# Performance work log

Measured on AMD Instinct MI355X. Metric: run time of the kernel, lower is better.

The kernel has to match this reference:

```python
import jax, jax.numpy as jnp
import numpy as np

EMBED = 1024
HEADS = 16
HEAD_DIM = EMBED // HEADS
B, S = 4, 1024


def setup_inputs() -> dict:
    key = jax.random.key(0)
    ks = jax.random.split(key, 8)
    return {
        "values": jax.random.normal(ks[0], (B, S, EMBED), dtype=jnp.float32),
        "keys": jax.random.normal(ks[1], (B, S, EMBED), dtype=jnp.float32),
        "query": jax.random.normal(ks[2], (B, S, EMBED), dtype=jnp.float32),
        "mask": jax.random.randint(ks[3], (B, 1, S, S), 0, 2, dtype=jnp.int32),
        "Wv": jax.random.normal(ks[4], (HEAD_DIM, HEAD_DIM), dtype=jnp.float32) / np.sqrt(HEAD_DIM),
        "Wq": jax.random.normal(ks[5], (HEAD_DIM, HEAD_DIM), dtype=jnp.float32) / np.sqrt(HEAD_DIM),
        "Wk": jax.random.normal(ks[6], (HEAD_DIM, HEAD_DIM), dtype=jnp.float32) / np.sqrt(HEAD_DIM),
        "Wu": jax.random.normal(ks[7], (EMBED, EMBED), dtype=jnp.float32) / np.sqrt(EMBED),
        "bu": jnp.zeros((EMBED,), dtype=jnp.float32),
    }


def reference(values, keys, query, mask, Wv, Wq, Wk, Wu, bu):
    n, s, _ = query.shape
    # split heads: [B, S, H, D]
    v = values.reshape(n, s, HEADS, HEAD_DIM)
    k = keys.reshape(n, s, HEADS, HEAD_DIM)
    q = query.reshape(n, s, HEADS, HEAD_DIM)
    # per-head linear (shared weight across heads); torch Linear: x @ W.T
    v = jnp.einsum("nshd,ed->nshe", v, Wv)
    k = jnp.einsum("nshd,ed->nshe", k, Wk)
    q = jnp.einsum("nshd,ed->nshe", q, Wq)
    # scores: [B, H, Q, K]
    dot = jnp.einsum("nqhd,nkhd->nhqk", q, k)
    dot = jnp.where(mask == 0, jnp.float32(-1e20), dot)
    # NOTE: original scales by sqrt(embed_size), not sqrt(head_dim)
    attn = jax.nn.softmax(dot / jnp.sqrt(jnp.float32(EMBED)), axis=3)
    out = jnp.einsum("nhql,nlhd->nqhd", attn, v)
    out = out.reshape(n, s, EMBED)
    return out @ Wu.T + bu
```

## Files before the change

kernel.cpp:

```cpp
#include <hip/hip_runtime.h>
#include <hip/hip_bf16.h>

#define EMBED 1024
#define HEADS 16
#define HDIM  64
#define BATCH 4
#define SEQ   1024

typedef __attribute__((ext_vector_type(8))) short  short8;
typedef __attribute__((ext_vector_type(4))) short  short4v;
typedef __attribute__((ext_vector_type(4))) float  float4v;
typedef __attribute__((ext_vector_type(8))) float  float8;
typedef __attribute__((ext_vector_type(2))) __bf16 bf16x2;
typedef __attribute__((ext_vector_type(8))) __bf16 bf16x8;

static __device__ __forceinline__ short cvt1(float f) {
  return __builtin_bit_cast(short, (__bf16)f);
}

static __device__ __forceinline__ unsigned pkbf(float a, float b) {
  bf16x2 v; v[0] = (__bf16)a; v[1] = (__bf16)b;
  return __builtin_bit_cast(unsigned, v);
}

static __device__ __forceinline__ float ex2(float x) {
  return __builtin_amdgcn_exp2f(x);
}

static __device__ __forceinline__ short8 cvt8(const float* p) {
  float4v a = *(const float4v*)p;
  float4v b = *(const float4v*)(p + 4);
  float8 f = __builtin_shufflevector(a, b, 0, 1, 2, 3, 4, 5, 6, 7);
  bf16x8 bb = __builtin_convertvector(f, bf16x8);
  return __builtin_bit_cast(short8, bb);
}

static __device__ __forceinline__ void block_sync_lds() {
  __builtin_amdgcn_sched_barrier(0);
  asm volatile("s_waitcnt lgkmcnt(0)" ::: "memory");
  __builtin_amdgcn_s_barrier();
  __builtin_amdgcn_sched_barrier(0);
}

#define QSCL 0.04508422002778011f

__global__ __launch_bounds__(256) void k_pre(
    const float* __restrict__ values, const float* __restrict__ keys,
    const float* __restrict__ query,
    const float* __restrict__ Wv, const float* __restrict__ Wq,
    const float* __restrict__ Wk, const float* __restrict__ Wu,
    const int* __restrict__ mask,
    short* __restrict__ qp, short* __restrict__ kp, short* __restrict__ vpT,
    unsigned char* __restrict__ maskb, short* __restrict__ wub) {
  const int b = blockIdx.x;
  const int t = threadIdx.x;
  if (b < 768) {
    const int l = t & 63, lr = l & 15, g = l >> 4;
    const int wbase = (b * 4 + (t >> 6)) * 4;
    const int z = wbase >> 12;
    const float* in_; const float* Wm;
    if (z == 0)      { in_ = query;  Wm = Wq; }
    else if (z == 1) { in_ = keys;   Wm = Wk; }
    else             { in_ = values; Wm = Wv; }
    const float scl = (z == 0) ? QSCL : 1.0f;

    short8 af0[4], af1[4];
    int hh[4], rr[4];
#pragma unroll
    for (int uu = 0; uu < 4; ++uu) {
      const int rem = (wbase + uu) & 4095;
      hh[uu] = rem & 15;
      rr[uu] = (rem >> 4) * 16;
      af0[uu] = cvt8(in_ + (size_t)(rr[uu] + lr) * EMBED + hh[uu] * HDIM + g * 8);
      af1[uu] = cvt8(in_ + (size_t)(rr[uu] + lr) * EMBED + hh[uu] * HDIM + 32 + g * 8);
    }
    short8 wf0[4], wf1[4];
#pragma unroll
    for (int nt = 0; nt < 4; ++nt) {
      wf0[nt] = cvt8(Wm + (size_t)(nt * 16 + lr) * HDIM + g * 8);
      wf1[nt] = cvt8(Wm + (size_t)(nt * 16 + lr) * HDIM + 32 + g * 8);
    }

#pragma unroll
    for (int uu = 0; uu < 4; ++uu) {
      const int h = hh[uu], r0 = rr[uu];
      const int n = r0 >> 10, s0 = r0 & 1023;
      const int nh = n * HEADS + h;
      float4v acc[4];
#pragma unroll
      for (int nt = 0; nt < 4; ++nt) {
        acc[nt] = (float4v){0.f, 0.f, 0.f, 0.f};
        acc[nt] = __builtin_amdgcn_mfma_f32_16x16x32_bf16(af0[uu], wf0[nt], acc[nt], 0, 0, 0);
        acc[nt] = __builtin_amdgcn_mfma_f32_16x16x32_bf16(af1[uu], wf1[nt], acc[nt], 0, 0, 0);
      }
      if (z == 2) {
#pragma unroll
        for (int nt = 0; nt < 4; ++nt) {
          short4v r;
          r[0]=cvt1(acc[nt][0]); r[1]=cvt1(acc[nt][1]);
          r[2]=cvt1(acc[nt][2]); r[3]=cvt1(acc[nt][3]);
          *(short4v*)(vpT + (size_t)(nh * HDIM + nt * 16 + lr) * SEQ + s0 + g * 4) = r;
        }
      } else {
        short* outp = (z == 0) ? qp : kp;
        const int b8 = ((s0 >> 4) & 1) * 8;
        const int rbase = s0 & ~31;
#pragma unroll
        for (int nt = 0; nt < 4; ++nt)
#pragma unroll
          for (int i = 0; i < 4; ++i) {
            const int row = (z == 0)
                ? (s0 + g * 4 + i)
                : (rbase + (g & 1) * 16 + b8 + (g >> 1) * 4 + i);
            outp[(size_t)(nh * SEQ + row) * HDIM + nt * 16 + lr] =
                cvt1(acc[nt][i] * scl);
          }
      }
    }
  } else if (b < 1280) {
    const int q0 = ((b - 768) * 8) * 256 + t;
#pragma unroll
    for (int it = 0; it < 8; ++it) {
      const int q = q0 + it * 256;
      uint4 v = *(const uint4*)(mask + (size_t)q * 4);
      unsigned nib = (v.x ? 1u : 0u) | (v.y ? 2u : 0u) |
                     (v.z ? 4u : 0u) | (v.w ? 8u : 0u);
      maskb[q] = (unsigned char)nib;
    }
  } else {
    const int base = (b - 1280) * 256 + t;
#pragma unroll
    for (int it = 0; it < 16; ++it) {
      int i4 = (base + it * 16384) * 4;
      float4v v = *(const float4v*)(Wu + i4);
      short4v r; r[0]=cvt1(v[0]); r[1]=cvt1(v[1]); r[2]=cvt1(v[2]); r[3]=cvt1(v[3]);
      *(short4v*)(wub + i4) = r;
    }
  }
}

__global__ __launch_bounds__(256, 2) void k_attn(
    const short* __restrict__ qp, const short* __restrict__ kp,
    const short* __restrict__ vpT, const unsigned char* __restrict__ maskb,
    short* __restrict__ ao) {
  const int bid = blockIdx.x;
  const int work = (bid & 7) * 64 + (bid >> 3);
  const int qt = work & 7, grp = work >> 3;
  const int h = grp & 15, n = grp >> 4;

  const int t256 = threadIdx.x;
  const int w = t256 >> 6, l = t256 & 63, lr = l & 15, g = l >> 4;
  const int nh = n * HEADS + h;
  const int q00 = qt * 128 + w * 16;
  const short* qb  = qp  + (size_t)nh * SEQ * HDIM;
  const short* kbp = kp  + (size_t)nh * SEQ * HDIM;
  const short* vb  = vpT + (size_t)nh * HDIM * SEQ;
  const unsigned char* mb0 = maskb + (size_t)(n * SEQ + q00 + lr) * 256;

  __shared__ __align__(16) short kls0[4096], kls1[4096];
  __shared__ __align__(16) short vls0[4096], vls1[4096];

  const int s0 = t256, s1 = t256 + 256;
  const int r0s = s0 >> 3, c0s = s0 & 7, r1s = s1 >> 3, c1s = s1 & 7;
  const int ld0 = r0s * 64 + ((c0s ^ (r0s & 7)) << 3);
  const int ld1 = r1s * 64 + ((c1s ^ (r1s & 7)) << 3);

  const int e = lr & 7;
  const int base0 = lr * 64 + ((g ^ e) << 3);
  const int base1 = lr * 64 + (((4 + g) ^ e) << 3);

  short8 qf0[2], qf1[2];
#pragma unroll
  for (int x = 0; x < 2; ++x) {
    qf0[x] = *(const short8*)(qb + (q00 + x * 64 + lr) * HDIM + g * 8);
    qf1[x] = *(const short8*)(qb + (q00 + x * 64 + lr) * HDIM + 32 + g * 8);
  }

  const short8 ones8 = {0x3F80, 0x3F80, 0x3F80, 0x3F80,
                        0x3F80, 0x3F80, 0x3F80, 0x3F80};

  float4v acc[2][4];
  float4v lac[2];
#pragma unroll
  for (int x = 0; x < 2; ++x) {
    lac[x] = (float4v){0.f, 0.f, 0.f, 0.f};
#pragma unroll
    for (int dt = 0; dt < 4; ++dt) acc[x][dt] = (float4v){0.f, 0.f, 0.f, 0.f};
  }

  auto issue = [&](int tile, short8& K0, short8& K1, short8& V0, short8& V1) {
    const int kn = tile * 64;
    K0 = *(const short8*)(kbp + kn * 64 + s0 * 8);
    K1 = *(const short8*)(kbp + kn * 64 + s1 * 8);
    V0 = *(const short8*)(vb + (size_t)r0s * SEQ + kn + c0s * 8);
    V1 = *(const short8*)(vb + (size_t)r1s * SEQ + kn + c1s * 8);
  };
  auto publish = [&](short* Kd, short* Vd, short8 K0, short8 K1, short8 V0, short8 V1) {
    *(short8*)(Kd + ld0) = K0;
    *(short8*)(Kd + ld1) = K1;
    *(short8*)(Vd + ld0) = V0;
    *(short8*)(Vd + ld1) = V1;
  };
  auto tilec = [&](const short* Kb, const short* Vb, int t) {
    float4v sT[2][4];
#pragma unroll
    for (int a = 0; a < 4; ++a) {
      short8 kf0 = *(const short8*)(Kb + a * 1024 + base0);
      short8 kf1 = *(const short8*)(Kb + a * 1024 + base1);
#pragma unroll
      for (int x = 0; x < 2; ++x) {
        float4v z = (float4v){0.f, 0.f, 0.f, 0.f};
        z = __builtin_amdgcn_mfma_f32_16x16x32_bf16(kf0, qf0[x], z, 0, 0, 0);
        sT[x][a] = __builtin_amdgcn_mfma_f32_16x16x32_bf16(kf1, qf1[x], z, 0, 0, 0);
      }
    }
    short8 pw0[2], pw1[2];
#pragma unroll
    for (int x = 0; x < 2; ++x) {
      uint4 mv = *(const uint4*)(mb0 + (size_t)x * 64 * 256 + t * 16);
      const unsigned wl = (g & 2) ? mv.y : mv.x;
      const unsigned wh = (g & 2) ? mv.w : mv.z;
      const int sh = (g & 1) * 16;
      unsigned dw[8];
#pragma unroll
      for (int a = 0; a < 4; ++a) {
        unsigned ta = ((a & 2) ? wh : wl) >> (sh + (a & 1) * 8);
        float p0 = ex2(sT[x][a][0]); p0 = (ta & 1u) ? p0 : 0.f;
        float p1 = ex2(sT[x][a][1]); p1 = (ta & 2u) ? p1 : 0.f;
        float p2 = ex2(sT[x][a][2]); p2 = (ta & 4u) ? p2 : 0.f;
        float p3 = ex2(sT[x][a][3]); p3 = (ta & 8u) ? p3 : 0.f;
        dw[a * 2]     = pkbf(p0, p1);
        dw[a * 2 + 1] = pkbf(p2, p3);
      }
      __builtin_memcpy(&pw0[x], &dw[0], 16);
      __builtin_memcpy(&pw1[x], &dw[4], 16);
      lac[x] = __builtin_amdgcn_mfma_f32_16x16x32_bf16(ones8, pw0[x], lac[x], 0, 0, 0);
      lac[x] = __builtin_amdgcn_mfma_f32_16x16x32_bf16(ones8, pw1[x], lac[x], 0, 0, 0);
    }
#pragma unroll
    for (int dt = 0; dt < 4; ++dt) {
      short8 vf0 = *(const short8*)(Vb + dt * 1024 + base0);
      short8 vf1 = *(const short8*)(Vb + dt * 1024 + base1);
#pragma unroll
      for (int x = 0; x < 2; ++x) {
        acc[x][dt] = __builtin_amdgcn_mfma_f32_16x16x32_bf16(vf0, pw0[x], acc[x][dt], 0, 0, 0);
        acc[x][dt] = __builtin_amdgcn_mfma_f32_16x16x32_bf16(vf1, pw1[x], acc[x][dt], 0, 0, 0);
      }
    }
  };

  short8 aK0, aK1, aV0, aV1;
  short8 bK0, bK1, bV0, bV1;

  issue(0, aK0, aK1, aV0, aV1);
  publish(kls0, vls0, aK0, aK1, aV0, aV1);
  issue(1, bK0, bK1, bV0, bV1);
  block_sync_lds();

  for (int tp = 0; tp < 8; ++tp) {
    if (tp < 7) issue(2 * tp + 2, aK0, aK1, aV0, aV1);
    tilec(kls0, vls0, 2 * tp);
    publish(kls1, vls1, bK0, bK1, bV0, bV1);
    block_sync_lds();
    if (tp < 7) issue(2 * tp + 3, bK0, bK1, bV0, bV1);
    tilec(kls1, vls1, 2 * tp + 1);
    if (tp < 7) {
      publish(kls0, vls0, aK0, aK1, aV0, aV1);
      block_sync_lds();
    }
  }

#pragma unroll
  for (int x = 0; x < 2; ++x) {
    const float inv = 1.f / fmaxf(lac[x][0], 1e-35f);
    short* aorow = ao + (size_t)(n * SEQ + q00 + x * 64 + lr) * EMBED + h * HDIM;
#pragma unroll
    for (int dt = 0; dt < 4; ++dt) {
      short4v r;
      r[0] = cvt1(acc[x][dt][0] * inv);
      r[1] = cvt1(acc[x][dt][1] * inv);
      r[2] = cvt1(acc[x][dt][2] * inv);
      r[3] = cvt1(acc[x][dt][3] * inv);
      *(short4v*)(aorow + dt * 16 + g * 4) = r;
    }
  }
}

__global__ __launch_bounds__(256, 1) void k_gemm(
    const short* __restrict__ ao, const short* __restrict__ wub,
    const float* __restrict__ bu, float* __restrict__ out) {
  const int r0 = blockIdx.x * 128, c0 = blockIdx.y * 128;
  const int t = threadIdx.x;
  const int w = t >> 6, l = t & 63, lr = l & 15, g = l >> 4;
  const int wr = w >> 1, wc = w & 1;

  __shared__ __align__(16) short als[2][128 * 64];
  __shared__ __align__(16) short bls[2][128 * 64];

  int ldc[4];
  const short *agp[4], *bgp[4];
#pragma unroll
  for (int j = 0; j < 4; ++j) {
    const int c = t + 256 * j;
    const int row = c >> 3, c8 = c & 7;
    ldc[j] = row * 64 + ((c8 ^ (row & 7)) << 3);
    agp[j] = ao  + (size_t)(r0 + row) * EMBED + c8 * 8;
    bgp[j] = wub + (size_t)(c0 + row) * EMBED + c8 * 8;
  }

  int aoff[4][2], boff[4][2];
#pragma unroll
  for (int fr = 0; fr < 4; ++fr) {
    const int ra = wr * 64 + fr * 16 + lr;
#pragma unroll
    for (int kk = 0; kk < 2; ++kk)
      aoff[fr][kk] = ra * 64 + (((kk * 4 + g) ^ (ra & 7)) << 3);
  }
#pragma unroll
  for (int fc = 0; fc < 4; ++fc) {
    const int rb = wc * 64 + fc * 16 + lr;
#pragma unroll
    for (int kk = 0; kk < 2; ++kk)
      boff[fc][kk] = rb * 64 + (((kk * 4 + g) ^ (rb & 7)) << 3);
  }

  float4v acc[4][4];
#pragma unroll
  for (int fr = 0; fr < 4; ++fr)
#pragma unroll
    for (int fc = 0; fc < 4; ++fc) acc[fr][fc] = (float4v){0.f, 0.f, 0.f, 0.f};

  short8 sAa[4], sBa[4], sAb[4], sBb[4];

  auto issueg = [&](int step, short8* SA, short8* SB) {
    const int kb = step * 64;
#pragma unroll
    for (int j = 0; j < 4; ++j) {
      SA[j] = *(const short8*)(agp[j] + kb);
      SB[j] = *(const short8*)(bgp[j] + kb);
    }
  };
  auto publishg = [&](short* Ad, short* Bd, const short8* SA, const short8* SB) {
#pragma unroll
    for (int j = 0; j < 4; ++j) {
      *(short8*)(Ad + ldc[j]) = SA[j];
      *(short8*)(Bd + ldc[j]) = SB[j];
    }
  };
  auto stepc = [&](const short* Ab, const short* Bb) {
#pragma unroll
    for (int kk = 0; kk < 2; ++kk) {
      short8 bf[4];
#pragma unroll
      for (int fc = 0; fc < 4; ++fc)
        bf[fc] = *(const short8*)(Bb + boff[fc][kk]);
#pragma unroll
      for (int fr = 0; fr < 4; ++fr) {
        short8 af = *(const short8*)(Ab + aoff[fr][kk]);
#pragma unroll
        for (int fc = 0; fc < 4; ++fc)
          acc[fr][fc] = __builtin_amdgcn_mfma_f32_16x16x32_bf16(af, bf[fc], acc[fr][fc], 0, 0, 0);
      }
    }
  };

  issueg(0, sAa, sBa);
  publishg(&als[0][0], &bls[0][0], sAa, sBa);
  issueg(1, sAb, sBb);
  block_sync_lds();

  for (int tp = 0; tp < 8; ++tp) {
    if (tp < 7) issueg(2 * tp + 2, sAa, sBa);
    stepc(&als[0][0], &bls[0][0]);
    publishg(&als[1][0], &bls[1][0], sAb, sBb);
    block_sync_lds();
    if (tp < 7) issueg(2 * tp + 3, sAb, sBb);
    stepc(&als[1][0], &bls[1][0]);
    if (tp < 7) {
      publishg(&als[0][0], &bls[0][0], sAa, sBa);
      block_sync_lds();
    }
  }

#pragma unroll
  for (int fc = 0; fc < 4; ++fc) {
    const int col = c0 + wc * 64 + fc * 16 + lr;
    const float bv = bu[col];
#pragma unroll
    for (int fr = 0; fr < 4; ++fr)
#pragma unroll
      for (int i = 0; i < 4; ++i) {
        const int row = r0 + wr * 64 + fr * 16 + g * 4 + i;
        out[(size_t)row * EMBED + col] = acc[fr][fc][i] + bv;
      }
  }
}

extern "C" void kernel_launch(void* const* d_in, const int* in_sizes, int n_in,
                              void* d_out, int out_size, void* d_ws, size_t ws_size,
                              hipStream_t stream) {
  const float* values = (const float*)d_in[0];
  const float* keys   = (const float*)d_in[1];
  const float* query  = (const float*)d_in[2];
  const int*   mask   = (const int*)d_in[3];
  const float* Wv     = (const float*)d_in[4];
  const float* Wq     = (const float*)d_in[5];
  const float* Wk     = (const float*)d_in[6];
  const float* Wu     = (const float*)d_in[7];
  const float* bu     = (const float*)d_in[8];
  float* out = (float*)d_out;

  char* ws = (char*)d_ws;
  short* qp  = (short*)ws;
  short* kp  = qp + (1u << 22);
  short* vpT = kp + (1u << 22);
  short* ao  = vpT + (1u << 22);
  unsigned char* maskb = (unsigned char*)(ws + (32u << 20));
  short* wub = (short*)(ws + (36u << 20));

  k_pre<<<dim3(1344), 256, 0, stream>>>(values, keys, query, Wv, Wq, Wk, Wu,
                                        mask, qp, kp, vpT, maskb, wub);
  k_attn<<<dim3(512), 256, 0, stream>>>(qp, kp, vpT, maskb, ao);
  k_gemm<<<dim3(32, 8), 256, 0, stream>>>(ao, wub, bu, out);
}
```

Before: 74.15 us.

## Use four LDS buffers to halve barriers per tile pair in attention and GEMM

Both the attention and output GEMM kernels move from two shared-memory buffers to four. Each iteration issues global loads for two tiles, computes two tiles back to back, then publishes both and syncs once, so there is one barrier per tile pair instead of two. This roughly doubles LDS use. The attention kernel reaches 128KB per block at launch_bounds(256,2) and the GEMM 128KB, which may cut occupancy. Each iteration also holds more prefetched registers in flight.

```diff
diff --git a/kernel.cpp b/kernel.cpp
--- a/kernel.cpp
+++ b/kernel.cpp
@@ -157,8 +157,8 @@
   const short* vb  = vpT + (size_t)nh * HDIM * SEQ;
   const unsigned char* mb0 = maskb + (size_t)(n * SEQ + q00 + lr) * 256;
 
-  __shared__ __align__(16) short kls0[4096], kls1[4096];
-  __shared__ __align__(16) short vls0[4096], vls1[4096];
+  __shared__ __align__(16) short kls0[4096], kls1[4096], kls2[4096], kls3[4096];
+  __shared__ __align__(16) short vls0[4096], vls1[4096], vls2[4096], vls3[4096];
 
   const int s0 = t256, s1 = t256 + 256;
   const int r0s = s0 >> 3, c0s = s0 & 7, r1s = s1 >> 3, c1s = s1 & 7;
@@ -253,19 +253,29 @@
   short8 bK0, bK1, bV0, bV1;
 
   issue(0, aK0, aK1, aV0, aV1);
+  issue(1, bK0, bK1, bV0, bV1);
   publish(kls0, vls0, aK0, aK1, aV0, aV1);
-  issue(1, bK0, bK1, bV0, bV1);
+  publish(kls1, vls1, bK0, bK1, bV0, bV1);
   block_sync_lds();
 
   for (int tp = 0; tp < 8; ++tp) {
-    if (tp < 7) issue(2 * tp + 2, aK0, aK1, aV0, aV1);
-    tilec(kls0, vls0, 2 * tp);
-    publish(kls1, vls1, bK0, bK1, bV0, bV1);
-    block_sync_lds();
-    if (tp < 7) issue(2 * tp + 3, bK0, bK1, bV0, bV1);
-    tilec(kls1, vls1, 2 * tp + 1);
     if (tp < 7) {
-      publish(kls0, vls0, aK0, aK1, aV0, aV1);
+      issue(2 * tp + 2, aK0, aK1, aV0, aV1);
+      issue(2 * tp + 3, bK0, bK1, bV0, bV1);
+    }
+    const short* kE = (tp & 1) ? kls2 : kls0;
+    const short* vE = (tp & 1) ? vls2 : vls0;
+    const short* kO = (tp & 1) ? kls3 : kls1;
+    const short* vO = (tp & 1) ? vls3 : vls1;
+    tilec(kE, vE, 2 * tp);
+    tilec(kO, vO, 2 * tp + 1);
+    if (tp < 7) {
+      short* kEn = (tp & 1) ? kls0 : kls2;
+      short* vEn = (tp & 1) ? vls0 : vls2;
+      short* kOn = (tp & 1) ? kls1 : kls3;
+      short* vOn = (tp & 1) ? vls1 : vls3;
+      publish(kEn, vEn, aK0, aK1, aV0, aV1);
+      publish(kOn, vOn, bK0, bK1, bV0, bV1);
       block_sync_lds();
     }
   }
@@ -294,8 +304,8 @@
   const int w = t >> 6, l = t & 63, lr = l & 15, g = l >> 4;
   const int wr = w >> 1, wc = w & 1;
 
-  __shared__ __align__(16) short als[2][128 * 64];
-  __shared__ __align__(16) short bls[2][128 * 64];
+  __shared__ __align__(16) short als0[8192], als1[8192], als2[8192], als3[8192];
+  __shared__ __align__(16) short bls0[8192], bls1[8192], bls2[8192], bls3[8192];
 
   int ldc[4];
   const short *agp[4], *bgp[4];
@@ -365,19 +375,29 @@
   };
 
   issueg(0, sAa, sBa);
-  publishg(&als[0][0], &bls[0][0], sAa, sBa);
   issueg(1, sAb, sBb);
+  publishg(als0, bls0, sAa, sBa);
+  publishg(als1, bls1, sAb, sBb);
   block_sync_lds();
 
   for (int tp = 0; tp < 8; ++tp) {
-    if (tp < 7) issueg(2 * tp + 2, sAa, sBa);
-    stepc(&als[0][0], &bls[0][0]);
-    publishg(&als[1][0], &bls[1][0], sAb, sBb);
-    block_sync_lds();
-    if (tp < 7) issueg(2 * tp + 3, sAb, sBb);
-    stepc(&als[1][0], &bls[1][0]);
     if (tp < 7) {
-      publishg(&als[0][0], &bls[0][0], sAa, sBa);
+      issueg(2 * tp + 2, sAa, sBa);
+      issueg(2 * tp + 3, sAb, sBb);
+    }
+    const short* aE = (tp & 1) ? als2 : als0;
+    const short* bE = (tp & 1) ? bls2 : bls0;
+    const short* aO = (tp & 1) ? als3 : als1;
+    const short* bO = (tp & 1) ? bls3 : bls1;
+    stepc(aE, bE);
+    stepc(aO, bO);
+    if (tp < 7) {
+      short* aEn = (tp & 1) ? als0 : als2;
+      short* bEn = (tp & 1) ? bls0 : bls2;
+      short* aOn = (tp & 1) ? als1 : als3;
+      short* bOn = (tp & 1) ? bls1 : bls3;
+      publishg(aEn, bEn, sAa, sBa);
+      publishg(aOn, bOn, sAb, sBb);
       block_sync_lds();
     }
   }
```

Measured after the change: 76.22 us. 2.8% more time.
